# Optimization experiments

Hardware: AMD Instinct MI355X
Metric: run time of the kernel (lower is better)

## Reference

```python
import jax, jax.numpy as jnp
import numpy as np
import math

U = 1024      # units
H = 16        # num_head
DH = U // H   # units_head
B = 2
Q = 1024      # query length
M = 1024      # memory length
KL = M + Q    # key length
R = KL + 1    # relative positions length (rel-shift needs k_len+1)
EPS = 1e-7    # K.epsilon()


def setup_inputs() -> dict:
    key = jax.random.key(0)
    ks = jax.random.split(key, 11)
    f32 = jnp.float32
    return {
        "inputs": jax.random.normal(ks[0], (B, Q, U), f32),
        "content": jax.random.normal(ks[1], (B, Q, U), f32),
        "memories": jax.random.normal(ks[2], (B, M, U), f32),
        "relatives": jax.random.normal(ks[3], (B, R, U), f32),
        "segment_mat": jax.random.uniform(ks[4], (B, Q, KL, 2), f32),
        "segment_embed": jax.random.normal(ks[5], (2, U), f32) * 0.02,
        "bias_context": jax.random.normal(ks[6], (U,), f32) * 0.02,
        "bias_relative": jax.random.normal(ks[7], (U,), f32) * 0.02,
        "bias_segment": jax.random.normal(ks[8], (U,), f32) * 0.02,
        "permutation": jax.random.uniform(ks[9], (B, Q, KL), f32),
        "kernel": jax.random.normal(ks[10], (U, 5 * U), f32) * 0.02,
    }


def _heads(x):
    # [B, L, U] -> [B, H, L, DH]
    b, l, _ = x.shape
    return x.reshape(b, l, H, DH).transpose(0, 2, 1, 3)


def _rel_shift(x, klen):
    # Transformer-XL relative shift via reshape trick. x: [B, H, Q, R]
    b, h, q, r = x.shape
    x = x.reshape(b, h, r, q)[:, :, 1:, :].reshape(b, h, q, r - 1)
    return x[:, :, :, :klen]


def reference(inputs, content, memories, relatives, segment_mat, segment_embed,
              bias_context, bias_relative, bias_segment, permutation, kernel):
    k_q = kernel[:, :U]
    k_kv = kernel[:, U:3 * U]
    k_r = kernel[:, 3 * U:4 * U]
    k_o = kernel[:, 4 * U:5 * U]

    full = jnp.concatenate([memories, content], axis=1)          # [B, KL, U]
    w_q = inputs @ k_q                                           # [B, Q, U]
    w_kv = full @ k_kv                                           # [B, KL, 2U]
    w_r = relatives @ k_r                                        # [B, R, U]

    w_k = _heads(w_kv[..., :U])                                  # [B, H, KL, DH]
    w_v = _heads(w_kv[..., U:])                                  # [B, H, KL, DH]

    # content term
    q_c = _heads(w_q + bias_context)                             # [B, H, Q, DH]
    a_context = jnp.einsum('bhqd,bhkd->bhqk', q_c, w_k)

    # relative-position term with rel-shift
    q_r = _heads(w_q + bias_relative)
    w_r_h = _heads(w_r)                                          # [B, H, R, DH]
    a_relative = _rel_shift(jnp.einsum('bhqd,bhrd->bhqr', q_r, w_r_h), KL)

    # segment term
    q_s = _heads(w_q + bias_segment)                             # [B, H, Q, DH]
    seg_e = segment_embed.T.reshape(H, DH, 2)                    # [H, DH, 2]
    qs_seg = jnp.einsum('bhqd,hds->bhqs', q_s, seg_e)            # [B, H, Q, 2]
    a_segment = jnp.einsum('bqks,bhqs->bhqk', segment_mat, qs_seg)

    att = (a_context + a_relative + a_segment) / math.sqrt(DH)   # [B, H, Q, KL]
    e = jnp.exp(att - jnp.max(att, axis=-1, keepdims=True))
    e = e * permutation[:, None, :, :]
    att = e / (jnp.sum(e, axis=-1, keepdims=True) + EPS)

    out = jnp.einsum('bhqk,bhkd->bhqd', att, w_v)                # [B, H, Q, DH]
    out = out.transpose(0, 2, 1, 3).reshape(inputs.shape[0], Q, U)
    return out @ k_o                                             # [B, Q, U]
```

## Files before the change

### kernel.cpp

```cpp
#include <hip/hip_runtime.h>

typedef __bf16 bf16;
typedef unsigned short u16;
typedef unsigned int u32;
typedef __attribute__((ext_vector_type(8))) __bf16 bf16x8;
typedef __attribute__((ext_vector_type(4))) __bf16 bf16x4;
typedef __attribute__((ext_vector_type(4))) float f32x4;
typedef __attribute__((ext_vector_type(8))) float f32x8;

#define SWZ(r, s) (((r) << 3) + ((s) ^ ((r) & 7)))
#define GSW(r, s) (((r) << 2) + ((s) ^ (((r) >> 1) & 3)))

__device__ __forceinline__ f32x4 mfma16(bf16x8 a, bf16x8 b, f32x4 c) {
  return __builtin_amdgcn_mfma_f32_16x16x32_bf16(a, b, c, 0, 0, 0);
}
__device__ __forceinline__ void gld16(const void* g, void* l) {
  __builtin_amdgcn_global_load_lds((const __attribute__((address_space(1))) void*)g,
                                   (__attribute__((address_space(3))) void*)l, 16, 0, 0);
}

__global__ __launch_bounds__(256) void cvt_bf16(const float* __restrict__ s,
                                                bf16* __restrict__ d, int n) {
  int i = (blockIdx.x * 256 + threadIdx.x) * 4;
  if (i < n) {
    f32x4 v = *reinterpret_cast<const f32x4*>(s + i);
    *reinterpret_cast<bf16x4*>(d + i) = __builtin_convertvector(v, bf16x4);
  }
}

__global__ __launch_bounds__(256) void cvt_full(const float* __restrict__ mem,
                                                const float* __restrict__ cont,
                                                bf16* __restrict__ d) {
  size_t i = ((size_t)blockIdx.x * 256 + threadIdx.x) * 4;
  int row = (int)(i >> 10), col = (int)(i & 1023);
  int b = row >> 11, r = row & 2047;
  const float* src = (r < 1024)
      ? (mem  + (((size_t)(b << 10) + r)        << 10) + col)
      : (cont + (((size_t)(b << 10) + (r - 1024)) << 10) + col);
  f32x4 v = *reinterpret_cast<const f32x4*>(src);
  *reinterpret_cast<bf16x4*>(d + i) = __builtin_convertvector(v, bf16x4);
}

__global__ __launch_bounds__(256) void cvt_seg(const float* __restrict__ s,
                                               bf16* __restrict__ d) {
  size_t i = ((size_t)blockIdx.x * 256 + threadIdx.x) * 8;
  f32x8 v = *reinterpret_cast<const f32x8*>(s + i);
  *reinterpret_cast<bf16x8*>(d + i) = __builtin_convertvector(v, bf16x8);
}

__global__ __launch_bounds__(256) void kT_cvt(const float* __restrict__ K,
                                              bf16* __restrict__ KT) {
  __shared__ float t[64][68];
  const int n0 = blockIdx.x << 6, k0 = blockIdx.y << 6;
  for (int idx = threadIdx.x; idx < 1024; idx += 256) {
    int r = idx >> 4, c4 = (idx & 15) << 2;
    f32x4 v = *reinterpret_cast<const f32x4*>(K + (size_t)(k0 + r) * 5120 + n0 + c4);
    t[r][c4] = v.x; t[r][c4 + 1] = v.y; t[r][c4 + 2] = v.z; t[r][c4 + 3] = v.w;
  }
  __syncthreads();
  for (int idx = threadIdx.x; idx < 1024; idx += 256) {
    int r = idx >> 4, c4 = (idx & 15) << 2;
    bf16x4 o = { (bf16)t[c4][r], (bf16)t[c4 + 1][r], (bf16)t[c4 + 2][r], (bf16)t[c4 + 3][r] };
    *reinterpret_cast<bf16x4*>(KT + (size_t)(n0 + r) * 1024 + k0 + c4) = o;
  }
}

__global__ __launch_bounds__(256) void seg_proj(const bf16* __restrict__ w_q,
                                                const float* __restrict__ bias_s,
                                                const float* __restrict__ seg_embed,
                                                float* __restrict__ qs) {
  int idx = blockIdx.x * 256 + threadIdx.x;
  int q = idx & 1023, h = (idx >> 10) & 15, b = idx >> 14;
  const bf16* wp = w_q + (((size_t)(b << 10) + q) << 10) + (h << 6);
  const float* bp = bias_s + (h << 6);
  const float* e0 = seg_embed + (h << 6);
  const float* e1 = seg_embed + 1024 + (h << 6);
  float s0 = 0.f, s1 = 0.f;
#pragma unroll 8
  for (int d = 0; d < 64; ++d) {
    float v = (float)wp[d] + bp[d];
    s0 = fmaf(v, e0[d], s0);
    s1 = fmaf(v, e1[d], s1);
  }
  qs[((size_t)idx << 1) + 0] = s0;
  qs[((size_t)idx << 1) + 1] = s1;
}

template<int OUT_MODE>
__global__ __launch_bounds__(256) void gemm_mfma(const bf16* __restrict__ A,
                                                 const bf16* __restrict__ BT,
                                                 void* __restrict__ C0v,
                                                 void* __restrict__ C1v,
                                                 int Mrows, int splitN) {
  __shared__ bf16 As[4096];
  __shared__ bf16 Bs[4096];
  const int tid = threadIdx.x;
  const int m0 = blockIdx.y << 7, n0 = blockIdx.x << 7;
  const int l = tid & 63, w = tid >> 6;
  const int wm = (w >> 1) << 6, wn = (w & 1) << 6;
  const int lc = l & 15, l16 = l >> 4;
  f32x4 acc[4][4] = {};
  const int r0 = tid >> 2, r1 = r0 + 64;
  const int sq = tid & 3;
  const int g0 = (sq ^ ((r0 >> 1) & 3)) << 3;

  for (int k0 = 0; k0 < 1024; k0 += 32) {
    __syncthreads();
    gld16(A  + (size_t)(m0 + r0) * 1024 + k0 + g0, &As[tid << 3]);
    gld16(BT + (size_t)(n0 + r0) * 1024 + k0 + g0, &Bs[tid << 3]);
    gld16(A  + (size_t)(m0 + r1) * 1024 + k0 + g0, &As[(tid + 256) << 3]);
    gld16(BT + (size_t)(n0 + r1) * 1024 + k0 + g0, &Bs[(tid + 256) << 3]);
    __syncthreads();
    bf16x8 af[4], bfv[4];
#pragma unroll
    for (int m = 0; m < 4; ++m)
      af[m] = *reinterpret_cast<const bf16x8*>(&As[GSW(wm + (m << 4) + lc, l16) << 3]);
#pragma unroll
    for (int n = 0; n < 4; ++n)
      bfv[n] = *reinterpret_cast<const bf16x8*>(&Bs[GSW(wn + (n << 4) + lc, l16) << 3]);
#pragma unroll
    for (int m = 0; m < 4; ++m)
#pragma unroll
      for (int n = 0; n < 4; ++n)
        acc[m][n] = mfma16(af[m], bfv[n], acc[m][n]);
  }
#pragma unroll
  for (int m = 0; m < 4; ++m) {
    const int rbase = m0 + wm + (m << 4) + (l16 << 2);
#pragma unroll
    for (int n = 0; n < 4; ++n) {
      const int col = n0 + wn + (n << 4) + lc;
      const int cc = (col < splitN) ? col : (col - splitN);
      void* Cv = (col < splitN) ? C0v : C1v;
#pragma unroll
      for (int r = 0; r < 4; ++r) {
        const int row = rbase + r;
        if (row < Mrows) {
          const float v = acc[m][n][r];
          const size_t off = ((size_t)row << 10) + cc;
          if (OUT_MODE == 1)      ((bf16*)Cv)[off] = (bf16)v;
          else if (OUT_MODE == 0) ((float*)Cv)[off] = v;
          else                    ((float*)Cv)[off] += v;
        }
      }
    }
  }
}

#define OFFA 7
#define OFFB 0

__global__ __launch_bounds__(256) void attn_mfma(
    const bf16* __restrict__ w_q, const bf16* __restrict__ w_k,
    const bf16* __restrict__ w_v, const bf16* __restrict__ w_rh,
    const float* __restrict__ qs_seg, const bf16* __restrict__ seg_b,
    const float* __restrict__ perm, const float* __restrict__ bias_c,
    const float* __restrict__ bias_r, bf16* __restrict__ a_hi,
    bf16* __restrict__ a_lo) {
  const int id = blockIdx.x;
  const int h  = (id >> 3) & 15;
  const int cg = (id & 7) | ((id >> 7) << 3);
  const int qt = cg & 15, b = cg >> 4;
  const int qi0 = qt << 6;
  const int tid = threadIdx.x;
  const int w = tid >> 6, l = tid & 63;
  const int lc = l & 15, l16 = l >> 4;
  const int w16 = w << 4;
  const int myq = w16 + lc;

  __shared__ bf16 kt[2][32 * 64];
  __shared__ u16  vt[2][64 * 40];
  __shared__ bf16 wbc[128 * 64];
  __shared__ bf16 wb2[96 * 64];
  __shared__ u16  pl[64 * 40];
  __shared__ float ART[4 * 960];
  __shared__ float facw[64], lroww[64];

  auto stageK = [&](int buf, int kj) {
    int r = tid >> 3, s = tid & 7;
    gld16(w_k + ((size_t)((b << 11) + kj + r) << 10) + (h << 6) + ((s ^ (r & 7)) << 3),
          &kt[buf][tid << 3]);
  };
  auto stageWB = [&](int L0, int nrows, int OFF) {
    for (int base = 0; base < nrows; base += 32) {
      int r = (tid >> 3) + base, s = tid & 7;
      int L = L0 + r;
      int slot = (L + OFF) & 127;
      int grow = L > 2048 ? 2048 : L;
      gld16(w_rh + ((size_t)(b * 2049 + grow) << 10) + (h << 6) + ((s ^ (slot & 7)) << 3),
            &wbc[((slot << 3) | s) << 3]);
    }
  };
  auto stageWB2 = [&]() {
    for (int base = 0; base < 96; base += 32) {
      int r = (tid >> 3) + base, s = tid & 7;
      gld16(w_rh + ((size_t)(b * 2049 + r) << 10) + (h << 6) + ((s ^ (r & 7)) << 3),
            &wb2[((r << 3) | s) << 3]);
    }
  };
  const int kv2 = (tid & 15) << 1, d4 = ((tid >> 4) & 15) << 2, kw = tid & 15;
  auto loadV = [&](int kj, uint2& ra, uint2& rb) {
    const u16* vp = (const u16*)w_v + ((size_t)((b << 11) + kj + kv2) << 10) + (h << 6) + d4;
    ra = *reinterpret_cast<const uint2*>(vp);
    rb = *reinterpret_cast<const uint2*>(vp + 1024);
  };
  auto writeV = [&](int buf, uint2 ra, uint2 rb) {
    u32* vt32 = reinterpret_cast<u32*>(&vt[buf][0]);
    vt32[(d4 + 0) * 20 + kw] = (ra.x & 0xffffu) | (rb.x << 16);
    vt32[(d4 + 1) * 20 + kw] = (ra.x >> 16) | (rb.x & 0xffff0000u);
    vt32[(d4 + 2) * 20 + kw] = (ra.y & 0xffffu) | (rb.y << 16);
    vt32[(d4 + 3) * 20 + kw] = (ra.y >> 16) | (rb.y & 0xffff0000u);
  };
  const size_t qrowg = (size_t)((b << 10) + qi0 + myq);
  auto loadSP = [&](int kj, bf16x8& sA, bf16x8& sB, f32x4& pA, f32x4& pB) {
    const bf16* sp = seg_b + (qrowg * 2048 + kj + (l16 << 2)) * 2;
    sA = *reinterpret_cast<const bf16x8*>(sp);
    sB = *reinterpret_cast<const bf16x8*>(sp + 32);
    const float* pp = perm + qrowg * 2048 + kj + (l16 << 2);
    pA = *reinterpret_cast<const f32x4*>(pp);
    pB = *reinterpret_cast<const f32x4*>(pp + 16);
  };

  stageK(0, 0);
  stageWB(961 - qi0, 96, OFFA);
  uint2 ra0, rb0;
  loadV(0, ra0, rb0);
  bf16x8 segA_c, segB_c, segA_n = {}, segB_n = {};
  f32x4 pmA_c, pmB_c, pmA_n = {}, pmB_n = {};
  loadSP(0, segA_c, segB_c, pmA_c, pmB_c);

  const int dlo = l16 << 3;
  bf16x8 qcf0, qcf1, qrf0, qrf1, qrg0, qrg1;
  {
    const bf16* qb  = w_q + ((qrowg) << 10) + (h << 6);
    const int rq1 = (qi0 + myq + 1 > 1023) ? 1023 : qi0 + myq + 1;
    const bf16* qb1 = w_q + (((size_t)(b << 10) + rq1) << 10) + (h << 6);
    f32x8 bc0 = *reinterpret_cast<const f32x8*>(bias_c + (h << 6) + dlo);
    f32x8 bc1 = *reinterpret_cast<const f32x8*>(bias_c + (h << 6) + 32 + dlo);
    f32x8 br0 = *reinterpret_cast<const f32x8*>(bias_r + (h << 6) + dlo);
    f32x8 br1 = *reinterpret_cast<const f32x8*>(bias_r + (h << 6) + 32 + dlo);
    bf16x8 q0 = *reinterpret_cast<const bf16x8*>(qb + dlo);
    bf16x8 q1 = *reinterpret_cast<const bf16x8*>(qb + 32 + dlo);
    bf16x8 p0 = *reinterpret_cast<const bf16x8*>(qb1 + dlo);
    bf16x8 p1 = *reinterpret_cast<const bf16x8*>(qb1 + 32 + dlo);
    qcf0 = __builtin_convertvector(__builtin_convertvector(q0, f32x8) + bc0, bf16x8);
    qcf1 = __builtin_convertvector(__builtin_convertvector(q1, f32x8) + bc1, bf16x8);
    qrf0 = __builtin_convertvector(__builtin_convertvector(q0, f32x8) + br0, bf16x8);
    qrf1 = __builtin_convertvector(__builtin_convertvector(q1, f32x8) + br1, bf16x8);
    qrg0 = __builtin_convertvector(__builtin_convertvector(p0, f32x8) + br0, bf16x8);
    qrg1 = __builtin_convertvector(__builtin_convertvector(p1, f32x8) + br1, bf16x8);
  }
  const float* qp = qs_seg + ((((size_t)((b << 4) + h) << 10) + qi0 + myq) << 1);
  const float qs0 = qp[0], qs1 = qp[1];

  writeV(0, ra0, rb0);
  __syncthreads();

  float mrow = -1e30f, lrow = 0.f;
  f32x4 o[4] = {};
  const float SCL = 0.125f * 1.44269504f;
  int cur = 0;
  uint2 ra_n = {}, rb_n = {};

  for (int t = 0; t < 64; ++t) {
    const int kj = t << 5;
    const int rel0 = kj - qi0;
    const bool strad = (rel0 == 1024) | (rel0 == 1056);
    const bool mainB = (rel0 >= 1088);
    const int nxt = cur ^ 1;

    if (t < 63) {
      const int kjn = kj + 32, rel0n = rel0 + 32;
      stageK(nxt, kjn);
      if (rel0n == 1024) stageWB2();
      if (rel0n == 1120)      stageWB(32, 96, OFFB);
      else if (rel0n != 1088) {
        if (rel0n <= 1056) stageWB(rel0n + 1025, 32, OFFA);
        else               stageWB(rel0n - 1024, 32, OFFB);
      }
      loadV(kjn, ra_n, rb_n);
      loadSP(kjn, segA_n, segB_n, pmA_n, pmB_n);
    }

    f32x4 s0 = {0.f, 0.f, 0.f, 0.f}, s1 = {0.f, 0.f, 0.f, 0.f};
    {
      const bf16* ktc = kt[cur];
      bf16x8 a0 = *reinterpret_cast<const bf16x8*>(&ktc[SWZ(lc, l16) << 3]);
      bf16x8 a1 = *reinterpret_cast<const bf16x8*>(&ktc[SWZ(lc, l16 + 4) << 3]);
      s0 = mfma16(a0, qcf0, s0); s0 = mfma16(a1, qcf1, s0);
      a0 = *reinterpret_cast<const bf16x8*>(&ktc[SWZ(16 + lc, l16) << 3]);
      a1 = *reinterpret_cast<const bf16x8*>(&ktc[SWZ(16 + lc, l16 + 4) << 3]);
      s1 = mfma16(a0, qcf0, s1); s1 = mfma16(a1, qcf1, s1);
    }

    float relv[8];
    {
      const bf16x8 ar0 = mainB ? qrg0 : qrf0;
      const bf16x8 ar1 = mainB ? qrg1 : qrf1;
      const bool useWb2 = (rel0 == 1088);
      int sbase;
      if (!mainB)       sbase = (rel0 + 1016 - w16) & 127;
      else if (useWb2)  sbase = 48 - w16;
      else              sbase = (rel0 - 1040 - w16) & 127;
      const bf16* wbp = useWb2 ? wb2 : wbc;
#pragma unroll
      for (int bg = 0; bg < 3; ++bg) {
        int prow = sbase + (bg << 4) + lc;
        if (!useWb2) prow &= 127;
        bf16x8 w0 = *reinterpret_cast<const bf16x8*>(&wbp[SWZ(prow, l16) << 3]);
        bf16x8 w1 = *reinterpret_cast<const bf16x8*>(&wbp[SWZ(prow, l16 + 4) << 3]);
        f32x4 a_ = {0.f, 0.f, 0.f, 0.f};
        a_ = mfma16(ar0, w0, a_); a_ = mfma16(ar1, w1, a_);
        *reinterpret_cast<f32x4*>(&ART[w * 960 + ((bg << 4) + lc) * 20 + (l16 << 2)]) = a_;
      }
#pragma unroll
      for (int jj = 0; jj < 4; ++jj) {
        relv[jj]     = ART[w * 960 + (15 + (l16 << 2) + jj - lc) * 20 + lc];
        relv[4 + jj] = ART[w * 960 + (31 + (l16 << 2) + jj - lc) * 20 + lc];
      }
      if (strad) {
#pragma unroll
        for (int bg = 0; bg < 3; ++bg) {
          int srow = rel0 - 1040 - w16 + (bg << 4) + lc;
          srow = srow < 0 ? 0 : (srow > 95 ? 95 : srow);
          bf16x8 w0 = *reinterpret_cast<const bf16x8*>(&wb2[SWZ(srow, l16) << 3]);
          bf16x8 w1 = *reinterpret_cast<const bf16x8*>(&wb2[SWZ(srow, l16 + 4) << 3]);
          f32x4 a_ = {0.f, 0.f, 0.f, 0.f};
          a_ = mfma16(qrg0, w0, a_); a_ = mfma16(qrg1, w1, a_);
          *reinterpret_cast<f32x4*>(&ART[w * 960 + ((bg << 4) + lc) * 20 + (l16 << 2)]) = a_;
        }
#pragma unroll
        for (int jj = 0; jj < 4; ++jj) {
          const int jA = (l16 << 2) + jj, jB = 16 + jA;
          float rbA = ART[w * 960 + (15 + jA - lc) * 20 + lc];
          float rbB = ART[w * 960 + (15 + jB - lc) * 20 + lc];
          if (rel0 + jA - myq >= 1025) relv[jj] = rbA;
          if (rel0 + jB - myq >= 1025) relv[4 + jj] = rbB;
        }
      }
    }

    {
      f32x8 sgA = __builtin_convertvector(segA_c, f32x8);
      f32x8 sgB = __builtin_convertvector(segB_c, f32x8);
      float sv[8];
#pragma unroll
      for (int jj = 0; jj < 4; ++jj) {
        sv[jj]     = (s0[jj] + relv[jj]     + sgA[2 * jj] * qs0 + sgA[2 * jj + 1] * qs1) * SCL;
        sv[4 + jj] = (s1[jj] + relv[4 + jj] + sgB[2 * jj] * qs0 + sgB[2 * jj + 1] * qs1) * SCL;
      }
      float tm = sv[0];
#pragma unroll
      for (int jj = 1; jj < 8; ++jj) tm = fmaxf(tm, sv[jj]);
      tm = fmaxf(tm, __shfl_xor(tm, 16));
      tm = fmaxf(tm, __shfl_xor(tm, 32));
      const float mn2 = fmaxf(mrow, tm);
      const float facr = exp2f(mrow - mn2);
      float e[8], rs = 0.f;
#pragma unroll
      for (int jj = 0; jj < 4; ++jj) {
        e[jj]     = exp2f(sv[jj] - mn2) * pmA_c[jj];
        e[4 + jj] = exp2f(sv[4 + jj] - mn2) * pmB_c[jj];
        rs += e[jj] + e[4 + jj];
      }
      rs += __shfl_xor(rs, 16);
      rs += __shfl_xor(rs, 32);
      mrow = mn2;
      lrow = lrow * facr + rs;
      bf16x4 pa, pb;
#pragma unroll
      for (int jj = 0; jj < 4; ++jj) { pa[jj] = (bf16)e[jj]; pb[jj] = (bf16)e[4 + jj]; }
      *reinterpret_cast<bf16x4*>(&pl[myq * 40 + (l16 << 2)]) = pa;
      *reinterpret_cast<bf16x4*>(&pl[myq * 40 + 16 + (l16 << 2)]) = pb;
      if (l16 == 0) facw[myq] = facr;
    }

    {
      float fr[4];
#pragma unroll
      for (int r = 0; r < 4; ++r) fr[r] = facw[w16 + (l16 << 2) + r];
#pragma unroll
      for (int n = 0; n < 4; ++n)
#pragma unroll
        for (int r = 0; r < 4; ++r) o[n][r] *= fr[r];
      bf16x8 ap = *reinterpret_cast<const bf16x8*>(&pl[(w16 + lc) * 40 + (l16 << 3)]);
#pragma unroll
      for (int n = 0; n < 4; ++n) {
        bf16x8 bv = *reinterpret_cast<const bf16x8*>(&vt[cur][((n << 4) + lc) * 40 + (l16 << 3)]);
        o[n] = mfma16(ap, bv, o[n]);
      }
    }

    if (t < 63) {
      writeV(nxt, ra_n, rb_n);
      segA_c = segA_n; segB_c = segB_n; pmA_c = pmA_n; pmB_c = pmB_n;
    }
    __syncthreads();
    cur = nxt;
  }

  if (l16 == 0) lroww[myq] = lrow;
  {
    float inv[4];
#pragma unroll
    for (int r = 0; r < 4; ++r)
      inv[r] = 1.f / (lroww[w16 + (l16 << 2) + r] + 1e-7f);
#pragma unroll
    for (int n = 0; n < 4; ++n) {
#pragma unroll
      for (int r = 0; r < 4; ++r) {
        const int row = qi0 + w16 + (l16 << 2) + r;
        const float v = o[n][r] * inv[r];
        const bf16 hi = (bf16)v;
        const float lof = v - (float)hi;
        const size_t off = (((size_t)(b << 10) + row) << 10) + (h << 6) + (n << 4) + lc;
        a_hi[off] = hi;
        a_lo[off] = (bf16)lof;
      }
    }
  }
}

extern "C" void kernel_launch(void* const* d_in, const int* in_sizes, int n_in,
                              void* d_out, int out_size, void* d_ws, size_t ws_size,
                              hipStream_t stream) {
  (void)in_sizes; (void)n_in; (void)out_size; (void)ws_size;
  const float* inputs    = (const float*)d_in[0];
  const float* content   = (const float*)d_in[1];
  const float* memories  = (const float*)d_in[2];
  const float* relatives = (const float*)d_in[3];
  const float* seg_mat   = (const float*)d_in[4];
  const float* seg_embed = (const float*)d_in[5];
  const float* bias_c    = (const float*)d_in[6];
  const float* bias_r    = (const float*)d_in[7];
  const float* bias_s    = (const float*)d_in[8];
  const float* perm      = (const float*)d_in[9];
  const float* kern      = (const float*)d_in[10];
  float* out = (float*)d_out;

  char* ws = (char*)d_ws;
  bf16*  in_b   = (bf16*)(ws);
  bf16*  full_b = (bf16*)(ws + 4194304);
  bf16*  rel_b  = (bf16*)(ws + 12582912);
  bf16*  kT     = (bf16*)(ws + 21233664);
  bf16*  w_q    = (bf16*)(ws + 31719424);
  bf16*  w_k    = (bf16*)(ws + 35913728);
  bf16*  w_v    = (bf16*)(ws + 44302336);
  bf16*  w_rh   = (bf16*)(ws + 52690944);
  bf16*  a_hi   = (bf16*)(ws + 61083648);
  float* qs     = (float*)(ws + 65277952);
  bf16*  seg_b  = (bf16*)(ws);
  bf16*  a_lo   = (bf16*)(ws + 16777216);

  dim3 blk(256);
  cvt_bf16<<<2048, blk, 0, stream>>>(inputs, in_b, 2097152);
  cvt_full<<<4096, blk, 0, stream>>>(memories, content, full_b);
  cvt_bf16<<<4098, blk, 0, stream>>>(relatives, rel_b, 4196352);
  kT_cvt<<<dim3(80, 16), blk, 0, stream>>>(kern, kT);

  gemm_mfma<1><<<dim3(8, 16),  blk, 0, stream>>>(in_b,   kT,           w_q,  w_q, 2048, 1 << 30);
  gemm_mfma<1><<<dim3(16, 32), blk, 0, stream>>>(full_b, kT + 1048576, w_k,  w_v, 4096, 1024);
  gemm_mfma<1><<<dim3(8, 33),  blk, 0, stream>>>(rel_b,  kT + 3145728, w_rh, w_rh, 4098, 1 << 30);
  seg_proj<<<128, blk, 0, stream>>>(w_q, bias_s, seg_embed, qs);
  cvt_seg<<<4096, blk, 0, stream>>>(seg_mat, seg_b);

  attn_mfma<<<512, blk, 0, stream>>>(w_q, w_k, w_v, w_rh, qs, seg_b, perm,
                                     bias_c, bias_r, a_hi, a_lo);

  gemm_mfma<0><<<dim3(8, 16), blk, 0, stream>>>(a_hi, kT + 4194304, out, out, 2048, 1 << 30);
  gemm_mfma<2><<<dim3(8, 16), blk, 0, stream>>>(a_lo, kT + 4194304, out, out, 2048, 1 << 30);
}
```

Baseline: 297.9 us.

## Fuse prep/projection launches, merge hi/lo output GEMM, add MFMA priority hints

Merges the conversion kernels and the kernel transpose into one launch. The three projection GEMMs now run as one launch, with a 64-row tile for the Q and relative projections, and the segment conversion and projection share one kernel. The attention output hi/lo parts are written interleaved into one K=2048 buffer, so a single output GEMM replaces the second pass that re-read and accumulated into the output. In attention, LDS fragment loads are hoisted ahead of the MFMA groups, which are wrapped in s_setprio. The aim is to cut launch overhead, tail effects and the read-modify-write of the output. The cost is branchy fused kernels and a workspace region reused for the concatenated activations.

Measured after the change: 269.3 us. 1.11x faster.

```diff
diff --git a/kernel.cpp b/kernel.cpp
--- a/kernel.cpp
+++ b/kernel.cpp
@@ -19,113 +19,86 @@
                                    (__attribute__((address_space(3))) void*)l, 16, 0, 0);
 }
 
-__global__ __launch_bounds__(256) void cvt_bf16(const float* __restrict__ s,
-                                                bf16* __restrict__ d, int n) {
-  int i = (blockIdx.x * 256 + threadIdx.x) * 4;
-  if (i < n) {
-    f32x4 v = *reinterpret_cast<const f32x4*>(s + i);
-    *reinterpret_cast<bf16x4*>(d + i) = __builtin_convertvector(v, bf16x4);
-  }
-}
-
-__global__ __launch_bounds__(256) void cvt_full(const float* __restrict__ mem,
-                                                const float* __restrict__ cont,
-                                                bf16* __restrict__ d) {
-  size_t i = ((size_t)blockIdx.x * 256 + threadIdx.x) * 4;
-  int row = (int)(i >> 10), col = (int)(i & 1023);
-  int b = row >> 11, r = row & 2047;
-  const float* src = (r < 1024)
-      ? (mem  + (((size_t)(b << 10) + r)        << 10) + col)
-      : (cont + (((size_t)(b << 10) + (r - 1024)) << 10) + col);
-  f32x4 v = *reinterpret_cast<const f32x4*>(src);
-  *reinterpret_cast<bf16x4*>(d + i) = __builtin_convertvector(v, bf16x4);
-}
-
-__global__ __launch_bounds__(256) void cvt_seg(const float* __restrict__ s,
-                                               bf16* __restrict__ d) {
-  size_t i = ((size_t)blockIdx.x * 256 + threadIdx.x) * 8;
-  f32x8 v = *reinterpret_cast<const f32x8*>(s + i);
-  *reinterpret_cast<bf16x8*>(d + i) = __builtin_convertvector(v, bf16x8);
-}
-
-__global__ __launch_bounds__(256) void kT_cvt(const float* __restrict__ K,
-                                              bf16* __restrict__ KT) {
+__global__ __launch_bounds__(256) void prep_all(
+    const float* __restrict__ inputs, const float* __restrict__ mem,
+    const float* __restrict__ cont, const float* __restrict__ rel,
+    const float* __restrict__ K, bf16* __restrict__ in_b,
+    bf16* __restrict__ full_b, bf16* __restrict__ rel_b, bf16* __restrict__ KT) {
   __shared__ float t[64][68];
-  const int n0 = blockIdx.x << 6, k0 = blockIdx.y << 6;
-  for (int idx = threadIdx.x; idx < 1024; idx += 256) {
-    int r = idx >> 4, c4 = (idx & 15) << 2;
-    f32x4 v = *reinterpret_cast<const f32x4*>(K + (size_t)(k0 + r) * 5120 + n0 + c4);
-    t[r][c4] = v.x; t[r][c4 + 1] = v.y; t[r][c4 + 2] = v.z; t[r][c4 + 3] = v.w;
-  }
-  __syncthreads();
-  for (int idx = threadIdx.x; idx < 1024; idx += 256) {
-    int r = idx >> 4, c4 = (idx & 15) << 2;
-    bf16x4 o = { (bf16)t[c4][r], (bf16)t[c4 + 1][r], (bf16)t[c4 + 2][r], (bf16)t[c4 + 3][r] };
-    *reinterpret_cast<bf16x4*>(KT + (size_t)(n0 + r) * 1024 + k0 + c4) = o;
-  }
-}
-
-__global__ __launch_bounds__(256) void seg_proj(const bf16* __restrict__ w_q,
-                                                const float* __restrict__ bias_s,
-                                                const float* __restrict__ seg_embed,
-                                                float* __restrict__ qs) {
-  int idx = blockIdx.x * 256 + threadIdx.x;
-  int q = idx & 1023, h = (idx >> 10) & 15, b = idx >> 14;
-  const bf16* wp = w_q + (((size_t)(b << 10) + q) << 10) + (h << 6);
-  const float* bp = bias_s + (h << 6);
-  const float* e0 = seg_embed + (h << 6);
-  const float* e1 = seg_embed + 1024 + (h << 6);
-  float s0 = 0.f, s1 = 0.f;
-#pragma unroll 8
-  for (int d = 0; d < 64; ++d) {
-    float v = (float)wp[d] + bp[d];
-    s0 = fmaf(v, e0[d], s0);
-    s1 = fmaf(v, e1[d], s1);
-  }
-  qs[((size_t)idx << 1) + 0] = s0;
-  qs[((size_t)idx << 1) + 1] = s1;
-}
-
-template<int OUT_MODE>
-__global__ __launch_bounds__(256) void gemm_mfma(const bf16* __restrict__ A,
-                                                 const bf16* __restrict__ BT,
-                                                 void* __restrict__ C0v,
-                                                 void* __restrict__ C1v,
-                                                 int Mrows, int splitN) {
-  __shared__ bf16 As[4096];
-  __shared__ bf16 Bs[4096];
-  const int tid = threadIdx.x;
-  const int m0 = blockIdx.y << 7, n0 = blockIdx.x << 7;
+  const int bid = blockIdx.x, tid = threadIdx.x;
+  if (bid < 1024) {
+    size_t i = ((size_t)bid * 256 + tid) * 8;
+    f32x8 v = *reinterpret_cast<const f32x8*>(inputs + i);
+    *reinterpret_cast<bf16x8*>(in_b + i) = __builtin_convertvector(v, bf16x8);
+  } else if (bid < 3072) {
+    size_t i = ((size_t)(bid - 1024) * 256 + tid) * 8;
+    int row = (int)(i >> 10), col = (int)(i & 1023);
+    int b = row >> 11, r = row & 2047;
+    const float* src = (r < 1024)
+        ? (mem  + (((size_t)(b << 10) + r)          << 10) + col)
+        : (cont + (((size_t)(b << 10) + (r - 1024)) << 10) + col);
+    f32x8 v = *reinterpret_cast<const f32x8*>(src);
+    *reinterpret_cast<bf16x8*>(full_b + i) = __builtin_convertvector(v, bf16x8);
+  } else if (bid < 5121) {
+    size_t i = ((size_t)(bid - 3072) * 256 + tid) * 8;
+    f32x8 v = *reinterpret_cast<const f32x8*>(rel + i);
+    *reinterpret_cast<bf16x8*>(rel_b + i) = __builtin_convertvector(v, bf16x8);
+  } else {
+    const int r = bid - 5121;
+    const int n0 = (r % 80) << 6, k0 = (r / 80) << 6;
+    for (int idx = tid; idx < 1024; idx += 256) {
+      int rr = idx >> 4, c4 = (idx & 15) << 2;
+      f32x4 v = *reinterpret_cast<const f32x4*>(K + (size_t)(k0 + rr) * 5120 + n0 + c4);
+      t[rr][c4] = v.x; t[rr][c4 + 1] = v.y; t[rr][c4 + 2] = v.z; t[rr][c4 + 3] = v.w;
+    }
+    __syncthreads();
+    for (int idx = tid; idx < 1024; idx += 256) {
+      int rr = idx >> 4, c4 = (idx & 15) << 2;
+      bf16x4 o = { (bf16)t[c4][rr], (bf16)t[c4 + 1][rr], (bf16)t[c4 + 2][rr], (bf16)t[c4 + 3][rr] };
+      *reinterpret_cast<bf16x4*>(KT + (size_t)(n0 + rr) * 1024 + k0 + c4) = o;
+    }
+  }
+}
+
+template<int MT, int OUT_MODE, int KLEN, bool KWRAP>
+__device__ __forceinline__ void gemm_body(
+    const bf16* __restrict__ A, const bf16* __restrict__ BT,
+    void* __restrict__ C0v, void* __restrict__ C1v,
+    int m0, int n0, int Mrows, int splitN, bf16* As, bf16* Bs, int tid) {
   const int l = tid & 63, w = tid >> 6;
-  const int wm = (w >> 1) << 6, wn = (w & 1) << 6;
+  const int wn = (w & 1) << 6;
+  const int wm = (w >> 1) * (MT / 2);
+  constexpr int MFR = MT / 32;
   const int lc = l & 15, l16 = l >> 4;
-  f32x4 acc[4][4] = {};
-  const int r0 = tid >> 2, r1 = r0 + 64;
+  f32x4 acc[MFR][4] = {};
+  const int r0 = tid >> 2;
   const int sq = tid & 3;
   const int g0 = (sq ^ ((r0 >> 1) & 3)) << 3;
 
-  for (int k0 = 0; k0 < 1024; k0 += 32) {
+  for (int k0 = 0; k0 < KLEN; k0 += 32) {
+    const int kk = KWRAP ? (k0 & 1023) : k0;
     __syncthreads();
-    gld16(A  + (size_t)(m0 + r0) * 1024 + k0 + g0, &As[tid << 3]);
-    gld16(BT + (size_t)(n0 + r0) * 1024 + k0 + g0, &Bs[tid << 3]);
-    gld16(A  + (size_t)(m0 + r1) * 1024 + k0 + g0, &As[(tid + 256) << 3]);
-    gld16(BT + (size_t)(n0 + r1) * 1024 + k0 + g0, &Bs[(tid + 256) << 3]);
+    gld16(A  + (size_t)(m0 + r0) * KLEN + k0 + g0, &As[tid << 3]);
+    gld16(BT + (size_t)(n0 + r0) * 1024 + kk + g0, &Bs[tid << 3]);
+    if (MT == 128)
+      gld16(A + (size_t)(m0 + r0 + 64) * KLEN + k0 + g0, &As[(tid + 256) << 3]);
+    gld16(BT + (size_t)(n0 + r0 + 64) * 1024 + kk + g0, &Bs[(tid + 256) << 3]);
     __syncthreads();
-    bf16x8 af[4], bfv[4];
-#pragma unroll
-    for (int m = 0; m < 4; ++m)
+    bf16x8 af[MFR], bfv[4];
+#pragma unroll
+    for (int m = 0; m < MFR; ++m)
       af[m] = *reinterpret_cast<const bf16x8*>(&As[GSW(wm + (m << 4) + lc, l16) << 3]);
 #pragma unroll
     for (int n = 0; n < 4; ++n)
       bfv[n] = *reinterpret_cast<const bf16x8*>(&Bs[GSW(wn + (n << 4) + lc, l16) << 3]);
 #pragma unroll
-    for (int m = 0; m < 4; ++m)
+    for (int m = 0; m < MFR; ++m)
 #pragma unroll
       for (int n = 0; n < 4; ++n)
         acc[m][n] = mfma16(af[m], bfv[n], acc[m][n]);
   }
 #pragma unroll
-  for (int m = 0; m < 4; ++m) {
+  for (int m = 0; m < MFR; ++m) {
     const int rbase = m0 + wm + (m << 4) + (l16 << 2);
 #pragma unroll
     for (int n = 0; n < 4; ++n) {
@@ -138,12 +111,71 @@
         if (row < Mrows) {
           const float v = acc[m][n][r];
           const size_t off = ((size_t)row << 10) + cc;
-          if (OUT_MODE == 1)      ((bf16*)Cv)[off] = (bf16)v;
-          else if (OUT_MODE == 0) ((float*)Cv)[off] = v;
-          else                    ((float*)Cv)[off] += v;
+          if (OUT_MODE == 1) ((bf16*)Cv)[off] = (bf16)v;
+          else               ((float*)Cv)[off] = v;
         }
       }
     }
+  }
+}
+
+__global__ __launch_bounds__(256) void proj_fused(
+    const bf16* __restrict__ in_b, const bf16* __restrict__ full_b,
+    const bf16* __restrict__ rel_b, const bf16* __restrict__ kT,
+    bf16* __restrict__ w_q, bf16* __restrict__ w_k, bf16* __restrict__ w_v,
+    bf16* __restrict__ w_rh) {
+  __shared__ bf16 As[4096];
+  __shared__ bf16 Bs[4096];
+  const int bid = blockIdx.x, tid = threadIdx.x;
+  if (bid < 256) {
+    gemm_body<64, 1, 1024, false>(in_b, kT, w_q, w_q,
+                                  (bid >> 3) << 6, (bid & 7) << 7, 2048, 1 << 30, As, Bs, tid);
+  } else if (bid < 768) {
+    const int r = bid - 256;
+    gemm_body<128, 1, 1024, false>(full_b, kT + (1 << 20), w_k, w_v,
+                                   (r >> 4) << 7, (r & 15) << 7, 4096, 1024, As, Bs, tid);
+  } else {
+    const int r = bid - 768;
+    gemm_body<64, 1, 1024, false>(rel_b, kT + 3 * (1 << 20), w_rh, w_rh,
+                                  (r >> 3) << 6, (r & 7) << 7, 4098, 1 << 30, As, Bs, tid);
+  }
+}
+
+__global__ __launch_bounds__(256) void out_proj(
+    const bf16* __restrict__ a_cat, const bf16* __restrict__ kTo,
+    float* __restrict__ out) {
+  __shared__ bf16 As[4096];
+  __shared__ bf16 Bs[4096];
+  const int bid = blockIdx.x, tid = threadIdx.x;
+  gemm_body<64, 0, 2048, true>(a_cat, kTo, out, out,
+                               (bid >> 3) << 6, (bid & 7) << 7, 2048, 1 << 30, As, Bs, tid);
+}
+
+__global__ __launch_bounds__(256) void mid_prep(
+    const float* __restrict__ seg_mat, bf16* __restrict__ seg_b,
+    const bf16* __restrict__ w_q, const float* __restrict__ bias_s,
+    const float* __restrict__ seg_embed, float* __restrict__ qs) {
+  const int bid = blockIdx.x, tid = threadIdx.x;
+  if (bid < 4096) {
+    size_t i = ((size_t)bid * 256 + tid) * 8;
+    f32x8 v = *reinterpret_cast<const f32x8*>(seg_mat + i);
+    *reinterpret_cast<bf16x8*>(seg_b + i) = __builtin_convertvector(v, bf16x8);
+  } else {
+    int idx = (bid - 4096) * 256 + tid;
+    int q = idx & 1023, h = (idx >> 10) & 15, b = idx >> 14;
+    const bf16* wp = w_q + (((size_t)(b << 10) + q) << 10) + (h << 6);
+    const float* bp = bias_s + (h << 6);
+    const float* e0 = seg_embed + (h << 6);
+    const float* e1 = seg_embed + 1024 + (h << 6);
+    float s0 = 0.f, s1 = 0.f;
+#pragma unroll 8
+    for (int d = 0; d < 64; ++d) {
+      float v = (float)wp[d] + bp[d];
+      s0 = fmaf(v, e0[d], s0);
+      s1 = fmaf(v, e1[d], s1);
+    }
+    qs[((size_t)idx << 1) + 0] = s0;
+    qs[((size_t)idx << 1) + 1] = s1;
   }
 }
 
@@ -155,8 +187,7 @@
     const bf16* __restrict__ w_v, const bf16* __restrict__ w_rh,
     const float* __restrict__ qs_seg, const bf16* __restrict__ seg_b,
     const float* __restrict__ perm, const float* __restrict__ bias_c,
-    const float* __restrict__ bias_r, bf16* __restrict__ a_hi,
-    bf16* __restrict__ a_lo) {
+    const float* __restrict__ bias_r, bf16* __restrict__ a_cat) {
   const int id = blockIdx.x;
   const int h  = (id >> 3) & 15;
   const int cg = (id & 7) | ((id >> 7) << 3);
@@ -287,10 +318,12 @@
       const bf16* ktc = kt[cur];
       bf16x8 a0 = *reinterpret_cast<const bf16x8*>(&ktc[SWZ(lc, l16) << 3]);
       bf16x8 a1 = *reinterpret_cast<const bf16x8*>(&ktc[SWZ(lc, l16 + 4) << 3]);
+      bf16x8 a2 = *reinterpret_cast<const bf16x8*>(&ktc[SWZ(16 + lc, l16) << 3]);
+      bf16x8 a3 = *reinterpret_cast<const bf16x8*>(&ktc[SWZ(16 + lc, l16 + 4) << 3]);
+      __builtin_amdgcn_s_setprio(1);
       s0 = mfma16(a0, qcf0, s0); s0 = mfma16(a1, qcf1, s0);
-      a0 = *reinterpret_cast<const bf16x8*>(&ktc[SWZ(16 + lc, l16) << 3]);
-      a1 = *reinterpret_cast<const bf16x8*>(&ktc[SWZ(16 + lc, l16 + 4) << 3]);
-      s1 = mfma16(a0, qcf0, s1); s1 = mfma16(a1, qcf1, s1);
+      s1 = mfma16(a2, qcf0, s1); s1 = mfma16(a3, qcf1, s1);
+      __builtin_amdgcn_s_setprio(0);
     }
 
     float relv[8];
@@ -310,7 +343,9 @@
         bf16x8 w0 = *reinterpret_cast<const bf16x8*>(&wbp[SWZ(prow, l16) << 3]);
         bf16x8 w1 = *reinterpret_cast<const bf16x8*>(&wbp[SWZ(prow, l16 + 4) << 3]);
         f32x4 a_ = {0.f, 0.f, 0.f, 0.f};
+        __builtin_amdgcn_s_setprio(1);
         a_ = mfma16(ar0, w0, a_); a_ = mfma16(ar1, w1, a_);
+        __builtin_amdgcn_s_setprio(0);
         *reinterpret_cast<f32x4*>(&ART[w * 960 + ((bg << 4) + lc) * 20 + (l16 << 2)]) = a_;
       }
 #pragma unroll
@@ -384,11 +419,16 @@
 #pragma unroll
         for (int r = 0; r < 4; ++r) o[n][r] *= fr[r];
       bf16x8 ap = *reinterpret_cast<const bf16x8*>(&pl[(w16 + lc) * 40 + (l16 << 3)]);
-#pragma unroll
-      for (int n = 0; n < 4; ++n) {
-        bf16x8 bv = *reinterpret_cast<const bf16x8*>(&vt[cur][((n << 4) + lc) * 40 + (l16 << 3)]);
-        o[n] = mfma16(ap, bv, o[n]);
-      }
+      bf16x8 bv0 = *reinterpret_cast<const bf16x8*>(&vt[cur][(lc) * 40 + (l16 << 3)]);
+      bf16x8 bv1 = *reinterpret_cast<const bf16x8*>(&vt[cur][(16 + lc) * 40 + (l16 << 3)]);
+      bf16x8 bv2 = *reinterpret_cast<const bf16x8*>(&vt[cur][(32 + lc) * 40 + (l16 << 3)]);
+      bf16x8 bv3 = *reinterpret_cast<const bf16x8*>(&vt[cur][(48 + lc) * 40 + (l16 << 3)]);
+      __builtin_amdgcn_s_setprio(1);
+      o[0] = mfma16(ap, bv0, o[0]);
+      o[1] = mfma16(ap, bv1, o[1]);
+      o[2] = mfma16(ap, bv2, o[2]);
+      o[3] = mfma16(ap, bv3, o[3]);
+      __builtin_amdgcn_s_setprio(0);
     }
 
     if (t < 63) {
@@ -413,9 +453,9 @@
         const float v = o[n][r] * inv[r];
         const bf16 hi = (bf16)v;
         const float lof = v - (float)hi;
-        const size_t off = (((size_t)(b << 10) + row) << 10) + (h << 6) + (n << 4) + lc;
-        a_hi[off] = hi;
-        a_lo[off] = (bf16)lof;
+        const size_t off = (((size_t)(b << 10) + row) << 11) + (h << 6) + (n << 4) + lc;
+        a_cat[off] = hi;
+        a_cat[off + 1024] = (bf16)lof;
       }
     }
   }
@@ -447,26 +487,17 @@
   bf16*  w_k    = (bf16*)(ws + 35913728);
   bf16*  w_v    = (bf16*)(ws + 44302336);
   bf16*  w_rh   = (bf16*)(ws + 52690944);
-  bf16*  a_hi   = (bf16*)(ws + 61083648);
   float* qs     = (float*)(ws + 65277952);
   bf16*  seg_b  = (bf16*)(ws);
-  bf16*  a_lo   = (bf16*)(ws + 16777216);
+  bf16*  a_cat  = (bf16*)(ws + 21233664);
+  bf16*  kTo    = (bf16*)(ws + 29622272);
 
   dim3 blk(256);
-  cvt_bf16<<<2048, blk, 0, stream>>>(inputs, in_b, 2097152);
-  cvt_full<<<4096, blk, 0, stream>>>(memories, content, full_b);
-  cvt_bf16<<<4098, blk, 0, stream>>>(relatives, rel_b, 4196352);
-  kT_cvt<<<dim3(80, 16), blk, 0, stream>>>(kern, kT);
-
-  gemm_mfma<1><<<dim3(8, 16),  blk, 0, stream>>>(in_b,   kT,           w_q,  w_q, 2048, 1 << 30);
-  gemm_mfma<1><<<dim3(16, 32), blk, 0, stream>>>(full_b, kT + 1048576, w_k,  w_v, 4096, 1024);
-  gemm_mfma<1><<<dim3(8, 33),  blk, 0, stream>>>(rel_b,  kT + 3145728, w_rh, w_rh, 4098, 1 << 30);
-  seg_proj<<<128, blk, 0, stream>>>(w_q, bias_s, seg_embed, qs);
-  cvt_seg<<<4096, blk, 0, stream>>>(seg_mat, seg_b);
-
+  prep_all<<<6401, blk, 0, stream>>>(inputs, memories, content, relatives, kern,
+                                     in_b, full_b, rel_b, kT);
+  proj_fused<<<1288, blk, 0, stream>>>(in_b, full_b, rel_b, kT, w_q, w_k, w_v, w_rh);
+  mid_prep<<<4224, blk, 0, stream>>>(seg_mat, seg_b, w_q, bias_s, seg_embed, qs);
   attn_mfma<<<512, blk, 0, stream>>>(w_q, w_k, w_v, w_rh, qs, seg_b, perm,
-                                     bias_c, bias_r, a_hi, a_lo);
-
-  gemm_mfma<0><<<dim3(8, 16), blk, 0, stream>>>(a_hi, kT + 4194304, out, out, 2048, 1 << 30);
-  gemm_mfma<2><<<dim3(8, 16), blk, 0, stream>>>(a_lo, kT + 4194304, out, out, 2048, 1 << 30);
-}
+                                     bias_c, bias_r, a_cat);
+  out_proj<<<256, blk, 0, stream>>>(a_cat, kTo, out);
+}
```
